# Kernel tuning notes

Measured on AMD Instinct MI355X. Metric: run time of the kernel, lower is better.

## Reference

```python
import jax, jax.numpy as jnp
import numpy as np

B, S, D, H = 4, 2048, 1024, 16
DK = D // H


def setup_inputs() -> dict:
    key = jax.random.key(0)
    ks = jax.random.split(key, 12)
    std = 0.02
    inp = {
        "query": jax.random.normal(ks[0], (B, S, D), jnp.float32),
        "key": jax.random.normal(ks[1], (B, S, D), jnp.float32),
        "value": jax.random.normal(ks[2], (B, S, D), jnp.float32),
        "mask": jnp.ones((B, 1, 1, S), jnp.int32),
        "Wq": jax.random.normal(ks[3], (D, D), jnp.float32) * std,
        "bq": jnp.zeros((D,), jnp.float32),
        "Wk": jax.random.normal(ks[4], (D, D), jnp.float32) * std,
        "bk": jnp.zeros((D,), jnp.float32),
        "Wv": jax.random.normal(ks[5], (D, D), jnp.float32) * std,
        "bv": jnp.zeros((D,), jnp.float32),
        "Wo": jax.random.normal(ks[6], (D, D), jnp.float32) * std,
        "bo": jnp.zeros((D,), jnp.float32),
    }
    return inp


def reference(query, key, value, mask, Wq, bq, Wk, bk, Wv, bv, Wo, bo):
    # nn.Linear: x @ W.T + b; then split heads -> [B, H, S, DK]
    def proj(x, W, b):
        y = x @ W.T + b
        return y.reshape(B, S, H, DK).transpose(0, 2, 1, 3)

    q = proj(query, Wq, bq)
    k = proj(key, Wk, bk)
    v = proj(value, Wv, bv)

    scale = 1.0 / jnp.sqrt(jnp.asarray(DK, q.dtype))
    scores = jnp.einsum('bhqd,bhkd->bhqk', q, k) * scale  # [B,H,S,S]
    scores = jnp.where(mask == 0, jnp.asarray(-1e9, scores.dtype), scores)
    p_attn = jax.nn.softmax(scores, axis=-1)  # dropout p=0 -> identity
    ctx = jnp.einsum('bhqk,bhkd->bhqd', p_attn, v)
    ctx = ctx.transpose(0, 2, 1, 3).reshape(B, S, D)
    out = ctx @ Wo.T + bo
    return out
```

## Files before the change

### kernel.cpp

```cpp
#include <hip/hip_runtime.h>

#define BB 4
#define SS 2048
#define DD 1024
#define HH 16
#define DKC 64
#define MT (BB*SS)
#define NX (MT*DD)
#define NW (DD*DD)

typedef _Float16 f16x8 __attribute__((ext_vector_type(8)));
typedef _Float16 f16x4 __attribute__((ext_vector_type(4)));
typedef float f32x4 __attribute__((ext_vector_type(4)));
typedef int   i32x4 __attribute__((ext_vector_type(4)));

#define GLDS16(g, l)                                                         \
  __builtin_amdgcn_global_load_lds(                                          \
      (__attribute__((address_space(1))) void*)(g),                          \
      (__attribute__((address_space(3))) void*)(l), 16, 0, 0)

__global__ __launch_bounds__(256) void cvt_all(const float* __restrict__ xq,
                                               const float* __restrict__ xk,
                                               const float* __restrict__ xv,
                                               const float* __restrict__ wq,
                                               const float* __restrict__ wk,
                                               const float* __restrict__ wv,
                                               const float* __restrict__ wo,
                                               _Float16* __restrict__ dst) {
  size_t i = ((size_t)blockIdx.x * 256 + threadIdx.x) * 4;
  const float* src; size_t off;
  if (i < (size_t)NX)          { src = xq; off = i; }
  else if (i < (size_t)2*NX)   { src = xk; off = i - (size_t)NX; }
  else if (i < (size_t)3*NX)   { src = xv; off = i - (size_t)2*NX; }
  else {
    size_t j = i - (size_t)3*NX;
    if (j < (size_t)NW)        { src = wq; off = j; }
    else if (j < (size_t)2*NW) { src = wk; off = j - (size_t)NW; }
    else if (j < (size_t)3*NW) { src = wv; off = j - (size_t)2*NW; }
    else                       { src = wo; off = j - (size_t)3*NW; }
  }
  f32x4 f = *(const f32x4*)(src + off);
  f16x4 o;
#pragma unroll
  for (int j = 0; j < 4; ++j) o[j] = (_Float16)f[j];
  *(f16x4*)(dst + i) = o;
}

__global__ __launch_bounds__(256) void gemm_qkv(const _Float16* __restrict__ Xb,
                                                const _Float16* __restrict__ Wb,
                                                const float* __restrict__ b0,
                                                const float* __restrict__ b1,
                                                const float* __restrict__ b2,
                                                _Float16* __restrict__ Pj) {
  const int z = blockIdx.z;
  const _Float16* A = Xb + (size_t)z * MT * DD;
  const _Float16* W = Wb + (size_t)z * DD * DD;
  const float* bias = (z == 0) ? b0 : ((z == 1) ? b1 : b2);
  _Float16* out = Pj + (size_t)z * MT * DD;

  const int m0 = blockIdx.x * 128;
  const int n0 = blockIdx.y * 128;
  const int t = threadIdx.x;
  const int lane = t & 63;
  const int wave = t >> 6;
  const int q = lane >> 4, r = lane & 15;
  const int wm = (wave & 1) * 64, wn = (wave >> 1) * 64;

  __shared__ __align__(16) _Float16 sA[2][128 * 32];
  __shared__ __align__(16) _Float16 sB[2][128 * 32];

  f32x4 acc[4][4] = {};

  const int row0 = t >> 2;
  const int csw = (t & 3) ^ ((t >> 3) & 3);
  const int fsw = (r >> 1) & 3;

  auto stage = [&](int buf, int k0) {
#pragma unroll
    for (int i = 0; i < 2; ++i) {
      GLDS16(A + (size_t)(m0 + row0 + 64 * i) * DD + k0 + csw * 8,
             &sA[buf][(t + 256 * i) * 8]);
      GLDS16(W + (size_t)(n0 + row0 + 64 * i) * DD + k0 + csw * 8,
             &sB[buf][(t + 256 * i) * 8]);
    }
  };

  stage(0, 0);
  __syncthreads();

  int cur = 0;
  for (int k0 = 0; k0 < DD; k0 += 32) {
    if (k0 + 32 < DD) stage(cur ^ 1, k0 + 32);

    f16x8 af[4], bf[4];
#pragma unroll
    for (int x = 0; x < 4; ++x) {
      af[x] = *(const f16x8*)&sA[cur][(wm + x * 16 + r) * 32 + ((q ^ fsw) * 8)];
      bf[x] = *(const f16x8*)&sB[cur][(wn + x * 16 + r) * 32 + ((q ^ fsw) * 8)];
    }
#pragma unroll
    for (int mi = 0; mi < 4; ++mi)
#pragma unroll
      for (int ni = 0; ni < 4; ++ni)
        acc[mi][ni] = __builtin_amdgcn_mfma_f32_16x16x32_f16(af[mi], bf[ni], acc[mi][ni], 0, 0, 0);
    __syncthreads();
    cur ^= 1;
  }

  if (z == 2) {
#pragma unroll
    for (int ni = 0; ni < 4; ++ni) {
      int gn = n0 + wn + ni * 16 + r;
      float bv = bias[gn];
      int h = gn >> 6, dk = gn & 63;
#pragma unroll
      for (int mi = 0; mi < 4; ++mi) {
        int gm = m0 + wm + mi * 16 + q * 4;
        int bb = gm >> 11, s0 = gm & 2047;
        int kl = s0 & 63;
        int kap0 = (kl & 15) * 4 + (kl >> 4);
        size_t base = ((size_t)((bb * HH + h) * DKC + dk)) * SS + (s0 - kl);
#pragma unroll
        for (int rr = 0; rr < 4; ++rr)
          out[base + kap0 + rr * 4] = (_Float16)(acc[mi][ni][rr] + bv);
      }
    }
  } else {
#pragma unroll
    for (int ni = 0; ni < 4; ++ni) {
      int gn = n0 + wn + ni * 16 + r;
      float bv = bias[gn];
      int h = gn >> 6, dk = gn & 63;
#pragma unroll
      for (int mi = 0; mi < 4; ++mi) {
#pragma unroll
        for (int rr = 0; rr < 4; ++rr) {
          int gm = m0 + wm + mi * 16 + q * 4 + rr;
          int bb = gm >> 11, s = gm & 2047;
          out[((size_t)((bb * HH + h) * SS + s)) * DKC + dk] = (_Float16)(acc[mi][ni][rr] + bv);
        }
      }
    }
  }
}

__global__ __launch_bounds__(256) void attn(const _Float16* __restrict__ Pj,
                                            const int* __restrict__ mask,
                                            _Float16* __restrict__ Cx) {
  const int qt = blockIdx.x, h = blockIdx.y, bb = blockIdx.z;
  const size_t hoff = ((size_t)(bb * HH + h) * SS) * DKC;
  const _Float16* Qh  = Pj + hoff;
  const _Float16* Kh  = Pj + (size_t)MT * DD + hoff;
  const _Float16* Vth = Pj + (size_t)2 * MT * DD + hoff;
  _Float16* Ch = Cx + hoff;
  const int* mrow = mask + bb * SS;

  const int t = threadIdx.x, lane = t & 63, wave = t >> 6;
  const int q = lane >> 4, r = lane & 15;
  const int qrow0 = qt * 128 + wave * 32;

  __shared__ __align__(16) _Float16 sK[64 * 64];
  __shared__ __align__(16) _Float16 sVt[64 * 64];
  __shared__ __align__(16) _Float16 sP[4][32 * 64];
  __shared__ __align__(16) _Float16 sMBh[SS];

  {
    int i0 = t * 8;
    i32x4 m0v = *(const i32x4*)(mrow + i0);
    i32x4 m1v = *(const i32x4*)(mrow + i0 + 4);
    f16x8 bvv;
#pragma unroll
    for (int j = 0; j < 4; ++j) {
      bvv[j]     = m0v[j] ? (_Float16)0.0f : (_Float16)(-30000.0f);
      bvv[4 + j] = m1v[j] ? (_Float16)0.0f : (_Float16)(-30000.0f);
    }
    *(f16x8*)&sMBh[i0] = bvv;
  }

  f16x8 qf[2][2];
#pragma unroll
  for (int mi = 0; mi < 2; ++mi)
#pragma unroll
    for (int kk = 0; kk < 2; ++kk)
      qf[mi][kk] = *(const f16x8*)&Qh[(size_t)(qrow0 + mi * 16 + r) * DKC + kk * 32 + q * 8];

  float lst[2][4] = {};
  f32x4 oacc[2][4] = {};

  const float C2 = 0.125f * 1.44269504089f;

  const int srow0 = t >> 3, scc = t & 7;

  f16x8 kpre[2], vpre[2];
#pragma unroll
  for (int i = 0; i < 2; ++i) {
    int row = srow0 + 32 * i;
    kpre[i] = *(const f16x8*)(Kh + (size_t)row * DKC + scc * 8);
    vpre[i] = *(const f16x8*)(Vth + (size_t)row * SS + scc * 8);
  }

  for (int kt = 0; kt < SS; kt += 64) {
#pragma unroll
    for (int i = 0; i < 2; ++i) {
      int row = srow0 + 32 * i;
      *(f16x8*)&sK [row * 64 + ((scc ^ (row & 7)) << 3)] = kpre[i];
      *(f16x8*)&sVt[row * 64 + ((scc ^ (row & 7)) << 3)] = vpre[i];
    }
    __syncthreads();

    if (kt + 64 < SS) {
#pragma unroll
      for (int i = 0; i < 2; ++i) {
        int row = srow0 + 32 * i;
        kpre[i] = *(const f16x8*)(Kh + (size_t)(kt + 64 + row) * DKC + scc * 8);
        vpre[i] = *(const f16x8*)(Vth + (size_t)row * SS + kt + 64 + scc * 8);
      }
    }

    f32x4 sacc[2][4] = {};
#pragma unroll
    for (int kk = 0; kk < 2; ++kk) {
      f16x8 kb[4];
#pragma unroll
      for (int ni = 0; ni < 4; ++ni)
        kb[ni] = *(const f16x8*)&sK[(ni * 16 + r) * 64 + (((kk * 4 + q) ^ (r & 7)) << 3)];
      __builtin_amdgcn_s_setprio(1);
#pragma unroll
      for (int mi = 0; mi < 2; ++mi)
#pragma unroll
        for (int ni = 0; ni < 4; ++ni)
          sacc[mi][ni] = __builtin_amdgcn_mfma_f32_16x16x32_f16(qf[mi][kk], kb[ni], sacc[mi][ni], 0, 0, 0);
      __builtin_amdgcn_s_setprio(0);
    }

    float mb[4];
#pragma unroll
    for (int ni = 0; ni < 4; ++ni) mb[ni] = (float)sMBh[kt + ni * 16 + r];

#pragma unroll
    for (int mi = 0; mi < 2; ++mi) {
#pragma unroll
      for (int rr = 0; rr < 4; ++rr) {
        float pp[4];
#pragma unroll
        for (int ni = 0; ni < 4; ++ni)
          pp[ni] = __builtin_amdgcn_exp2f(__builtin_fmaf(sacc[mi][ni][rr], C2, mb[ni]));
        lst[mi][rr] += (pp[0] + pp[1]) + (pp[2] + pp[3]);
        int prow = mi * 16 + q * 4 + rr;
        int g = (r >> 1) ^ ((q * 4 + rr) & 7);
        int goff = prow * 64 + (g << 3) + ((r & 1) << 2);
        unsigned lo = __builtin_bit_cast(unsigned, __builtin_amdgcn_cvt_pkrtz(pp[0], pp[1]));
        unsigned hi = __builtin_bit_cast(unsigned, __builtin_amdgcn_cvt_pkrtz(pp[2], pp[3]));
        uint2 u; u.x = lo; u.y = hi;
        *(uint2*)&sP[wave][goff] = u;
      }
    }
    __threadfence_block();

#pragma unroll
    for (int kk = 0; kk < 2; ++kk) {
      f16x8 ap[2], vb[4];
#pragma unroll
      for (int mi = 0; mi < 2; ++mi)
        ap[mi] = *(const f16x8*)&sP[wave][(mi * 16 + r) * 64 + (((kk * 4 + q) ^ (r & 7)) << 3)];
#pragma unroll
      for (int ni = 0; ni < 4; ++ni)
        vb[ni] = *(const f16x8*)&sVt[(ni * 16 + r) * 64 + (((kk * 4 + q) ^ (r & 7)) << 3)];
      __builtin_amdgcn_s_setprio(1);
#pragma unroll
      for (int mi = 0; mi < 2; ++mi)
#pragma unroll
        for (int ni = 0; ni < 4; ++ni)
          oacc[mi][ni] = __builtin_amdgcn_mfma_f32_16x16x32_f16(ap[mi], vb[ni], oacc[mi][ni], 0, 0, 0);
      __builtin_amdgcn_s_setprio(0);
    }
    __syncthreads();
  }

#pragma unroll
  for (int mi = 0; mi < 2; ++mi)
#pragma unroll
    for (int rr = 0; rr < 4; ++rr) {
      float l = lst[mi][rr];
#pragma unroll
      for (int d = 1; d < 16; d <<= 1) l += __shfl_xor(l, d);
      lst[mi][rr] = 1.0f / l;
    }

#pragma unroll
  for (int mi = 0; mi < 2; ++mi)
#pragma unroll
    for (int ni = 0; ni < 4; ++ni)
#pragma unroll
      for (int rr = 0; rr < 4; ++rr) {
        int row = qrow0 + mi * 16 + q * 4 + rr;
        Ch[(size_t)row * DKC + ni * 16 + r] = (_Float16)(oacc[mi][ni][rr] * lst[mi][rr]);
      }
}

__global__ __launch_bounds__(256) void gemm_out(const _Float16* __restrict__ Cx,
                                                const _Float16* __restrict__ W,
                                                const float* __restrict__ bias,
                                                float* __restrict__ out) {
  const int m0 = blockIdx.x * 128;
  const int n0 = blockIdx.y * 128;
  const int t = threadIdx.x;
  const int lane = t & 63;
  const int wave = t >> 6;
  const int q = lane >> 4, r = lane & 15;
  const int wm = (wave & 1) * 64, wn = (wave >> 1) * 64;

  __shared__ __align__(16) _Float16 sA[2][128 * 32];
  __shared__ __align__(16) _Float16 sB[2][128 * 32];

  f32x4 acc[4][4] = {};

  const int row0 = t >> 2;
  const int csw = (t & 3) ^ ((t >> 3) & 3);
  const int fsw = (r >> 1) & 3;

  size_t abase[2];
#pragma unroll
  for (int i = 0; i < 2; ++i) {
    int gm = m0 + row0 + 64 * i;
    int bb = gm >> 11, s = gm & 2047;
    abase[i] = ((size_t)(bb * HH) * SS + s) * DKC;
  }

  auto stage = [&](int buf, int k0) {
    int head = k0 >> 6, off = (k0 & 63) + csw * 8;
#pragma unroll
    for (int i = 0; i < 2; ++i) {
      GLDS16(Cx + abase[i] + (size_t)head * SS * DKC + off,
             &sA[buf][(t + 256 * i) * 8]);
      GLDS16(W + (size_t)(n0 + row0 + 64 * i) * DD + k0 + csw * 8,
             &sB[buf][(t + 256 * i) * 8]);
    }
  };

  stage(0, 0);
  __syncthreads();

  int cur = 0;
  for (int k0 = 0; k0 < DD; k0 += 32) {
    if (k0 + 32 < DD) stage(cur ^ 1, k0 + 32);

    f16x8 af[4], bf[4];
#pragma unroll
    for (int x = 0; x < 4; ++x) {
      af[x] = *(const f16x8*)&sA[cur][(wm + x * 16 + r) * 32 + ((q ^ fsw) * 8)];
      bf[x] = *(const f16x8*)&sB[cur][(wn + x * 16 + r) * 32 + ((q ^ fsw) * 8)];
    }
#pragma unroll
    for (int mi = 0; mi < 4; ++mi)
#pragma unroll
      for (int ni = 0; ni < 4; ++ni)
        acc[mi][ni] = __builtin_amdgcn_mfma_f32_16x16x32_f16(af[mi], bf[ni], acc[mi][ni], 0, 0, 0);
    __syncthreads();
    cur ^= 1;
  }

#pragma unroll
  for (int ni = 0; ni < 4; ++ni) {
    int gn = n0 + wn + ni * 16 + r;
    float bv = bias[gn];
#pragma unroll
    for (int mi = 0; mi < 4; ++mi) {
#pragma unroll
      for (int rr = 0; rr < 4; ++rr) {
        int gm = m0 + wm + mi * 16 + q * 4 + rr;
        out[(size_t)gm * DD + gn] = acc[mi][ni][rr] + bv;
      }
    }
  }
}

extern "C" void kernel_launch(void* const* d_in, const int* in_sizes, int n_in,
                              void* d_out, int out_size, void* d_ws, size_t ws_size,
                              hipStream_t stream) {
  const float* query = (const float*)d_in[0];
  const float* key_  = (const float*)d_in[1];
  const float* value = (const float*)d_in[2];
  const int*   mask  = (const int*)d_in[3];
  const float* Wq = (const float*)d_in[4];
  const float* bq = (const float*)d_in[5];
  const float* Wk = (const float*)d_in[6];
  const float* bk = (const float*)d_in[7];
  const float* Wv = (const float*)d_in[8];
  const float* bv = (const float*)d_in[9];
  const float* Wo = (const float*)d_in[10];
  const float* bo = (const float*)d_in[11];
  float* out = (float*)d_out;

  _Float16* Xb = (_Float16*)d_ws;
  _Float16* Wb = Xb + (size_t)3 * NX;
  _Float16* Pj = Wb + (size_t)4 * NW;
  _Float16* Cx = Pj + (size_t)3 * NX;

  cvt_all<<<(3 * NX + 4 * NW) / 1024, 256, 0, stream>>>(query, key_, value, Wq, Wk, Wv, Wo, Xb);

  gemm_qkv<<<dim3(MT / 128, DD / 128, 3), 256, 0, stream>>>(Xb, Wb, bq, bk, bv, Pj);
  attn<<<dim3(SS / 128, HH, BB), 256, 0, stream>>>(Pj, mask, Cx);
  gemm_out<<<dim3(MT / 128, DD / 128), 256, 0, stream>>>(Cx, Wb + (size_t)3 * NW, bo, out);
}
```

Baseline: 363.6 us.

## Use register-prefetch GEMM staging, vectorized epilogues, and register-resident P in attention

Both GEMMs drop the double-buffered direct global-to-LDS loads for a register prefetch followed by a single-buffer LDS store. This halves the LDS footprint and may raise occupancy, at the cost of extra VGPRs and a sync per step. The QKV projection epilogues now write packed f16x4 vectors instead of scalar stores, so the K and V outputs use a new permuted layout. The attention kernel computes S^T (K as the A operand), so the softmax probabilities land in registers in the layout the PV MFMA needs. This removes the sP shared-memory round trip and its fence, and the row-sum reduction becomes two cross-lane shuffles plus a broadcast.

```diff
diff --git a/kernel.cpp b/kernel.cpp
--- a/kernel.cpp
+++ b/kernel.cpp
@@ -13,11 +13,7 @@
 typedef _Float16 f16x4 __attribute__((ext_vector_type(4)));
 typedef float f32x4 __attribute__((ext_vector_type(4)));
 typedef int   i32x4 __attribute__((ext_vector_type(4)));
-
-#define GLDS16(g, l)                                                         \
-  __builtin_amdgcn_global_load_lds(                                          \
-      (__attribute__((address_space(1))) void*)(g),                          \
-      (__attribute__((address_space(3))) void*)(l), 16, 0, 0)
+typedef unsigned u32x4 __attribute__((ext_vector_type(4)));
 
 __global__ __launch_bounds__(256) void cvt_all(const float* __restrict__ xq,
                                                const float* __restrict__ xk,
@@ -66,37 +62,43 @@
   const int q = lane >> 4, r = lane & 15;
   const int wm = (wave & 1) * 64, wn = (wave >> 1) * 64;
 
-  __shared__ __align__(16) _Float16 sA[2][128 * 32];
-  __shared__ __align__(16) _Float16 sB[2][128 * 32];
+  __shared__ __align__(16) _Float16 sA[128 * 32];
+  __shared__ __align__(16) _Float16 sB[128 * 32];
 
   f32x4 acc[4][4] = {};
 
-  const int row0 = t >> 2;
-  const int csw = (t & 3) ^ ((t >> 3) & 3);
+  const int row0 = t >> 2, cc = t & 3;
+  const int wch = (t & 3) ^ ((t >> 3) & 3);
   const int fsw = (r >> 1) & 3;
 
-  auto stage = [&](int buf, int k0) {
+  f16x8 apre[2], bpre[2];
+
+  auto prefetch = [&](int k0) {
 #pragma unroll
     for (int i = 0; i < 2; ++i) {
-      GLDS16(A + (size_t)(m0 + row0 + 64 * i) * DD + k0 + csw * 8,
-             &sA[buf][(t + 256 * i) * 8]);
-      GLDS16(W + (size_t)(n0 + row0 + 64 * i) * DD + k0 + csw * 8,
-             &sB[buf][(t + 256 * i) * 8]);
+      int row = row0 + 64 * i;
+      apre[i] = *(const f16x8*)(A + (size_t)(m0 + row) * DD + k0 + cc * 8);
+      bpre[i] = *(const f16x8*)(W + (size_t)(n0 + row) * DD + k0 + cc * 8);
     }
   };
 
-  stage(0, 0);
-  __syncthreads();
-
-  int cur = 0;
+  prefetch(0);
+
   for (int k0 = 0; k0 < DD; k0 += 32) {
-    if (k0 + 32 < DD) stage(cur ^ 1, k0 + 32);
+#pragma unroll
+    for (int i = 0; i < 2; ++i) {
+      int row = row0 + 64 * i;
+      *(f16x8*)&sA[row * 32 + wch * 8] = apre[i];
+      *(f16x8*)&sB[row * 32 + wch * 8] = bpre[i];
+    }
+    __syncthreads();
+    if (k0 + 32 < DD) prefetch(k0 + 32);
 
     f16x8 af[4], bf[4];
 #pragma unroll
     for (int x = 0; x < 4; ++x) {
-      af[x] = *(const f16x8*)&sA[cur][(wm + x * 16 + r) * 32 + ((q ^ fsw) * 8)];
-      bf[x] = *(const f16x8*)&sB[cur][(wn + x * 16 + r) * 32 + ((q ^ fsw) * 8)];
+      af[x] = *(const f16x8*)&sA[(wm + x * 16 + r) * 32 + ((q ^ fsw) * 8)];
+      bf[x] = *(const f16x8*)&sB[(wn + x * 16 + r) * 32 + ((q ^ fsw) * 8)];
     }
 #pragma unroll
     for (int mi = 0; mi < 4; ++mi)
@@ -104,41 +106,41 @@
       for (int ni = 0; ni < 4; ++ni)
         acc[mi][ni] = __builtin_amdgcn_mfma_f32_16x16x32_f16(af[mi], bf[ni], acc[mi][ni], 0, 0, 0);
     __syncthreads();
-    cur ^= 1;
   }
 
   if (z == 2) {
+    int s_tile = (m0 + wm) & 2047;
+    int bb2 = (m0 + wm) >> 11;
 #pragma unroll
     for (int ni = 0; ni < 4; ++ni) {
       int gn = n0 + wn + ni * 16 + r;
       float bv = bias[gn];
-      int h = gn >> 6, dk = gn & 63;
+      int hh = gn >> 6, dk = gn & 63;
+      size_t base = ((size_t)((bb2 * HH + hh) * DKC + dk)) * SS + s_tile;
 #pragma unroll
       for (int mi = 0; mi < 4; ++mi) {
-        int gm = m0 + wm + mi * 16 + q * 4;
-        int bb = gm >> 11, s0 = gm & 2047;
-        int kl = s0 & 63;
-        int kap0 = (kl & 15) * 4 + (kl >> 4);
-        size_t base = ((size_t)((bb * HH + h) * DKC + dk)) * SS + (s0 - kl);
-#pragma unroll
-        for (int rr = 0; rr < 4; ++rr)
-          out[base + kap0 + rr * 4] = (_Float16)(acc[mi][ni][rr] + bv);
+        int kap0 = 4 * (mi & 1) + 8 * q + 32 * (mi >> 1);
+        f16x4 o4;
+#pragma unroll
+        for (int rr = 0; rr < 4; ++rr) o4[rr] = (_Float16)(acc[mi][ni][rr] + bv);
+        *(f16x4*)&out[base + kap0] = o4;
       }
     }
   } else {
-#pragma unroll
-    for (int ni = 0; ni < 4; ++ni) {
-      int gn = n0 + wn + ni * 16 + r;
-      float bv = bias[gn];
-      int h = gn >> 6, dk = gn & 63;
-#pragma unroll
-      for (int mi = 0; mi < 4; ++mi) {
-#pragma unroll
-        for (int rr = 0; rr < 4; ++rr) {
-          int gm = m0 + wm + mi * 16 + q * 4 + rr;
-          int bb = gm >> 11, s = gm & 2047;
-          out[((size_t)((bb * HH + h) * SS + s)) * DKC + dk] = (_Float16)(acc[mi][ni][rr] + bv);
-        }
+    int hh = (n0 + wn) >> 6;
+    float bv4[4];
+#pragma unroll
+    for (int ni = 0; ni < 4; ++ni) bv4[ni] = bias[n0 + wn + ni * 16 + r];
+#pragma unroll
+    for (int mi = 0; mi < 4; ++mi) {
+#pragma unroll
+      for (int rr = 0; rr < 4; ++rr) {
+        int gm = m0 + wm + mi * 16 + q * 4 + rr;
+        int bb2 = gm >> 11, s = gm & 2047;
+        f16x4 o4;
+#pragma unroll
+        for (int ni = 0; ni < 4; ++ni) o4[ni] = (_Float16)(acc[mi][ni][rr] + bv4[ni]);
+        *(f16x4*)&out[((size_t)((bb2 * HH + hh) * SS + s)) * DKC + r * 4] = o4;
       }
     }
   }
@@ -161,7 +163,6 @@
 
   __shared__ __align__(16) _Float16 sK[64 * 64];
   __shared__ __align__(16) _Float16 sVt[64 * 64];
-  __shared__ __align__(16) _Float16 sP[4][32 * 64];
   __shared__ __align__(16) _Float16 sMBh[SS];
 
   {
@@ -179,12 +180,12 @@
 
   f16x8 qf[2][2];
 #pragma unroll
-  for (int mi = 0; mi < 2; ++mi)
+  for (int n = 0; n < 2; ++n)
 #pragma unroll
     for (int kk = 0; kk < 2; ++kk)
-      qf[mi][kk] = *(const f16x8*)&Qh[(size_t)(qrow0 + mi * 16 + r) * DKC + kk * 32 + q * 8];
-
-  float lst[2][4] = {};
+      qf[n][kk] = *(const f16x8*)&Qh[(size_t)(qrow0 + n * 16 + r) * DKC + kk * 32 + q * 8];
+
+  float lst[2] = {};
   f32x4 oacc[2][4] = {};
 
   const float C2 = 0.125f * 1.44269504089f;
@@ -217,75 +218,76 @@
       }
     }
 
-    f32x4 sacc[2][4] = {};
+    f32x4 sacc[4][2] = {};
 #pragma unroll
     for (int kk = 0; kk < 2; ++kk) {
       f16x8 kb[4];
 #pragma unroll
-      for (int ni = 0; ni < 4; ++ni)
-        kb[ni] = *(const f16x8*)&sK[(ni * 16 + r) * 64 + (((kk * 4 + q) ^ (r & 7)) << 3)];
+      for (int a = 0; a < 4; ++a)
+        kb[a] = *(const f16x8*)&sK[(a * 16 + r) * 64 + (((kk * 4 + q) ^ (r & 7)) << 3)];
       __builtin_amdgcn_s_setprio(1);
 #pragma unroll
-      for (int mi = 0; mi < 2; ++mi)
-#pragma unroll
-        for (int ni = 0; ni < 4; ++ni)
-          sacc[mi][ni] = __builtin_amdgcn_mfma_f32_16x16x32_f16(qf[mi][kk], kb[ni], sacc[mi][ni], 0, 0, 0);
+      for (int a = 0; a < 4; ++a)
+#pragma unroll
+        for (int n = 0; n < 2; ++n)
+          sacc[a][n] = __builtin_amdgcn_mfma_f32_16x16x32_f16(kb[a], qf[n][kk], sacc[a][n], 0, 0, 0);
       __builtin_amdgcn_s_setprio(0);
     }
 
-    float mb[4];
-#pragma unroll
-    for (int ni = 0; ni < 4; ++ni) mb[ni] = (float)sMBh[kt + ni * 16 + r];
-
-#pragma unroll
-    for (int mi = 0; mi < 2; ++mi) {
-#pragma unroll
-      for (int rr = 0; rr < 4; ++rr) {
+    f16x4 mbv[4];
+#pragma unroll
+    for (int a = 0; a < 4; ++a)
+      mbv[a] = *(const f16x4*)&sMBh[kt + a * 16 + q * 4];
+
+    unsigned pw[2][2][4];
+#pragma unroll
+    for (int n = 0; n < 2; ++n) {
+#pragma unroll
+      for (int a = 0; a < 4; ++a) {
         float pp[4];
 #pragma unroll
-        for (int ni = 0; ni < 4; ++ni)
-          pp[ni] = __builtin_amdgcn_exp2f(__builtin_fmaf(sacc[mi][ni][rr], C2, mb[ni]));
-        lst[mi][rr] += (pp[0] + pp[1]) + (pp[2] + pp[3]);
-        int prow = mi * 16 + q * 4 + rr;
-        int g = (r >> 1) ^ ((q * 4 + rr) & 7);
-        int goff = prow * 64 + (g << 3) + ((r & 1) << 2);
-        unsigned lo = __builtin_bit_cast(unsigned, __builtin_amdgcn_cvt_pkrtz(pp[0], pp[1]));
-        unsigned hi = __builtin_bit_cast(unsigned, __builtin_amdgcn_cvt_pkrtz(pp[2], pp[3]));
-        uint2 u; u.x = lo; u.y = hi;
-        *(uint2*)&sP[wave][goff] = u;
-      }
-    }
-    __threadfence_block();
+        for (int reg = 0; reg < 4; ++reg)
+          pp[reg] = __builtin_amdgcn_exp2f(__builtin_fmaf(sacc[a][n][reg], C2, (float)mbv[a][reg]));
+        lst[n] += (pp[0] + pp[1]) + (pp[2] + pp[3]);
+        pw[n][a >> 1][(a & 1) * 2]     = __builtin_bit_cast(unsigned, __builtin_amdgcn_cvt_pkrtz(pp[0], pp[1]));
+        pw[n][a >> 1][(a & 1) * 2 + 1] = __builtin_bit_cast(unsigned, __builtin_amdgcn_cvt_pkrtz(pp[2], pp[3]));
+      }
+    }
 
 #pragma unroll
     for (int kk = 0; kk < 2; ++kk) {
-      f16x8 ap[2], vb[4];
-#pragma unroll
-      for (int mi = 0; mi < 2; ++mi)
-        ap[mi] = *(const f16x8*)&sP[wave][(mi * 16 + r) * 64 + (((kk * 4 + q) ^ (r & 7)) << 3)];
+      f16x8 vb[4];
 #pragma unroll
       for (int ni = 0; ni < 4; ++ni)
         vb[ni] = *(const f16x8*)&sVt[(ni * 16 + r) * 64 + (((kk * 4 + q) ^ (r & 7)) << 3)];
       __builtin_amdgcn_s_setprio(1);
 #pragma unroll
-      for (int mi = 0; mi < 2; ++mi)
+      for (int n = 0; n < 2; ++n) {
+        u32x4 w = { pw[n][kk][0], pw[n][kk][1], pw[n][kk][2], pw[n][kk][3] };
+        f16x8 apn = __builtin_bit_cast(f16x8, w);
 #pragma unroll
         for (int ni = 0; ni < 4; ++ni)
-          oacc[mi][ni] = __builtin_amdgcn_mfma_f32_16x16x32_f16(ap[mi], vb[ni], oacc[mi][ni], 0, 0, 0);
+          oacc[n][ni] = __builtin_amdgcn_mfma_f32_16x16x32_f16(apn, vb[ni], oacc[n][ni], 0, 0, 0);
+      }
       __builtin_amdgcn_s_setprio(0);
     }
     __syncthreads();
   }
 
-#pragma unroll
-  for (int mi = 0; mi < 2; ++mi)
-#pragma unroll
-    for (int rr = 0; rr < 4; ++rr) {
-      float l = lst[mi][rr];
-#pragma unroll
-      for (int d = 1; d < 16; d <<= 1) l += __shfl_xor(l, d);
-      lst[mi][rr] = 1.0f / l;
-    }
+  float rinv[2];
+#pragma unroll
+  for (int n = 0; n < 2; ++n) {
+    float l = lst[n];
+    l += __shfl_xor(l, 16);
+    l += __shfl_xor(l, 32);
+    rinv[n] = 1.0f / l;
+  }
+  float rn[2][4];
+#pragma unroll
+  for (int n = 0; n < 2; ++n)
+#pragma unroll
+    for (int rr = 0; rr < 4; ++rr)
+      rn[n][rr] = __shfl(rinv[n], q * 4 + rr);
 
 #pragma unroll
   for (int mi = 0; mi < 2; ++mi)
@@ -294,7 +296,7 @@
 #pragma unroll
       for (int rr = 0; rr < 4; ++rr) {
         int row = qrow0 + mi * 16 + q * 4 + rr;
-        Ch[(size_t)row * DKC + ni * 16 + r] = (_Float16)(oacc[mi][ni][rr] * lst[mi][rr]);
+        Ch[(size_t)row * DKC + ni * 16 + r] = (_Float16)(oacc[mi][ni][rr] * rn[mi][rr]);
       }
 }
 
@@ -310,13 +312,13 @@
   const int q = lane >> 4, r = lane & 15;
   const int wm = (wave & 1) * 64, wn = (wave >> 1) * 64;
 
-  __shared__ __align__(16) _Float16 sA[2][128 * 32];
-  __shared__ __align__(16) _Float16 sB[2][128 * 32];
+  __shared__ __align__(16) _Float16 sA[128 * 32];
+  __shared__ __align__(16) _Float16 sB[128 * 32];
 
   f32x4 acc[4][4] = {};
 
-  const int row0 = t >> 2;
-  const int csw = (t & 3) ^ ((t >> 3) & 3);
+  const int row0 = t >> 2, cc = t & 3;
+  const int wch = (t & 3) ^ ((t >> 3) & 3);
   const int fsw = (r >> 1) & 3;
 
   size_t abase[2];
@@ -327,29 +329,34 @@
     abase[i] = ((size_t)(bb * HH) * SS + s) * DKC;
   }
 
-  auto stage = [&](int buf, int k0) {
-    int head = k0 >> 6, off = (k0 & 63) + csw * 8;
+  f16x8 apre[2], bpre[2];
+
+  auto prefetch = [&](int k0) {
+    int head = k0 >> 6, off = (k0 & 63) + cc * 8;
 #pragma unroll
     for (int i = 0; i < 2; ++i) {
-      GLDS16(Cx + abase[i] + (size_t)head * SS * DKC + off,
-             &sA[buf][(t + 256 * i) * 8]);
-      GLDS16(W + (size_t)(n0 + row0 + 64 * i) * DD + k0 + csw * 8,
-             &sB[buf][(t + 256 * i) * 8]);
+      apre[i] = *(const f16x8*)(Cx + abase[i] + (size_t)head * SS * DKC + off);
+      bpre[i] = *(const f16x8*)(W + (size_t)(n0 + row0 + 64 * i) * DD + k0 + cc * 8);
     }
   };
 
-  stage(0, 0);
-  __syncthreads();
-
-  int cur = 0;
+  prefetch(0);
+
   for (int k0 = 0; k0 < DD; k0 += 32) {
-    if (k0 + 32 < DD) stage(cur ^ 1, k0 + 32);
+#pragma unroll
+    for (int i = 0; i < 2; ++i) {
+      int row = row0 + 64 * i;
+      *(f16x8*)&sA[row * 32 + wch * 8] = apre[i];
+      *(f16x8*)&sB[row * 32 + wch * 8] = bpre[i];
+    }
+    __syncthreads();
+    if (k0 + 32 < DD) prefetch(k0 + 32);
 
     f16x8 af[4], bf[4];
 #pragma unroll
     for (int x = 0; x < 4; ++x) {
-      af[x] = *(const f16x8*)&sA[cur][(wm + x * 16 + r) * 32 + ((q ^ fsw) * 8)];
-      bf[x] = *(const f16x8*)&sB[cur][(wn + x * 16 + r) * 32 + ((q ^ fsw) * 8)];
+      af[x] = *(const f16x8*)&sA[(wm + x * 16 + r) * 32 + ((q ^ fsw) * 8)];
+      bf[x] = *(const f16x8*)&sB[(wn + x * 16 + r) * 32 + ((q ^ fsw) * 8)];
     }
 #pragma unroll
     for (int mi = 0; mi < 4; ++mi)
@@ -357,7 +364,6 @@
       for (int ni = 0; ni < 4; ++ni)
         acc[mi][ni] = __builtin_amdgcn_mfma_f32_16x16x32_f16(af[mi], bf[ni], acc[mi][ni], 0, 0, 0);
     __syncthreads();
-    cur ^= 1;
   }
 
 #pragma unroll
```

Result: faster. 346.7 us (-4.7%).
